# Kernel optimization log

Measured on AMD Instinct MI355X. Metric: run time of the kernel, lower is better.

The kernel has to match this reference:

```python
import jax, jax.numpy as jnp
import numpy as np
from jax import lax

S = 8  # down/up-sample factor


def _seg_means(x, z):
    """Directional running means between zero-boundaries along the last axis.

    x: float [..., L] values; z: bool [..., L], True at zero-boundary positions.
    For position t strictly between consecutive boundaries (prev, nxt):
      lr[t] = mean(x[prev:t+1]),  rl[t] = mean(x[t:nxt+1]); else keep x[t].
    """
    L = x.shape[-1]
    ar = jnp.arange(L)
    ax = x.ndim - 1
    # last zero index strictly before t (-1 if none)
    idx = jnp.where(z, ar, -1)
    prev = lax.cummax(idx, axis=ax)
    prev = jnp.concatenate(
        [jnp.full(prev.shape[:-1] + (1,), -1, prev.dtype), prev[..., :-1]], axis=-1)
    # first zero index strictly after t (L if none)
    idx2 = jnp.where(z, ar, L)
    nxt = lax.cummin(idx2, axis=ax, reverse=True)
    nxt = jnp.concatenate(
        [nxt[..., 1:], jnp.full(nxt.shape[:-1] + (1,), L, nxt.dtype)], axis=-1)
    valid = (~z) & (prev >= 0) & (nxt < L)
    # padded cumsum: cs0[..., k] = sum(x[..., :k]), length L+1
    cs0 = jnp.concatenate(
        [jnp.zeros(x.shape[:-1] + (1,), x.dtype), jnp.cumsum(x, axis=-1)], axis=-1)
    prev_c = jnp.clip(prev, 0, L - 1)
    nxt_c = jnp.clip(nxt, 0, L - 1)
    sum_lr = cs0[..., 1:] - jnp.take_along_axis(cs0, prev_c, axis=-1)   # x[prev..t]
    sum_rl = jnp.take_along_axis(cs0, nxt_c + 1, axis=-1) - cs0[..., :-1]  # x[t..nxt]
    cnt_lr = jnp.maximum(ar - prev + 1, 1).astype(x.dtype)
    cnt_rl = jnp.maximum(nxt - ar + 1, 1).astype(x.dtype)
    lr = jnp.where(valid, sum_lr / cnt_lr, x)
    rl = jnp.where(valid, sum_rl / cnt_rl, x)
    return lr, rl


def setup_inputs() -> dict:
    key = jax.random.key(0)
    k0, k1 = jax.random.split(key)
    N, C, H, W = 8, 1, 2048, 2048
    x0 = jax.random.normal(k0, (N, C, H, W), dtype=jnp.float32)
    x1 = jax.random.randint(k1, (N, C, H, W), 0, 8, dtype=jnp.int32)
    return {"x0": x0, "x1": x1}


def reference(x0, x1):
    # nearest-neighbor downsample by 8 (matches F.interpolate scale_factor=1/8, mode='nearest')
    x0d = x0[..., ::S, ::S]
    zd = (x1[..., ::S, ::S] == 0)
    # horizontal pass (along rows)
    xh_lr, xh_rl = _seg_means(x0d, zd)
    # vertical pass (along columns) via transpose
    xv_tb, xv_bt = _seg_means(jnp.swapaxes(x0d, -1, -2), jnp.swapaxes(zd, -1, -2))
    y = xh_lr + xh_rl + jnp.swapaxes(xv_tb, -1, -2) + jnp.swapaxes(xv_bt, -1, -2)
    # nearest-neighbor upsample by 8
    y = jnp.repeat(jnp.repeat(y, S, axis=-2), S, axis=-1)
    return y
```

## Files before the change

### kernel.cpp

```cpp
#include <hip/hip_runtime.h>

#define DS   256
#define FULL 2048
#define NIMG 8
#define CG   4

typedef float f32x4 __attribute__((ext_vector_type(4)));
typedef int   i32x4 __attribute__((ext_vector_type(4)));

__device__ __forceinline__ float seg_fast(float x, bool z, int j,
                                          float* s_cs,
                                          unsigned long long* s_msk,
                                          float* s_ws) {
    const int lane = j & 63;
    const int w    = j >> 6;
    unsigned long long m = __ballot(z);

    float s = x;
    #pragma unroll
    for (int off = 1; off < 64; off <<= 1) {
        float t = __shfl_up(s, off, 64);
        if (lane >= off) s += t;
    }
    if (lane == 63) s_ws[w]  = s;
    if (lane == 0)  s_msk[w] = m;
    __syncthreads();

    float pre = 0.f;
    for (int ww = 0; ww < w; ++ww) pre += s_ws[ww];
    s += pre;
    s_cs[j] = s;

    unsigned long long lo = m & ((1ULL << lane) - 1ULL);
    int prev = -1;
    if (lo) prev = (w << 6) + 63 - __builtin_clzll(lo);
    else {
        for (int ww = w - 1; ww >= 0; --ww) {
            unsigned long long mm = s_msk[ww];
            if (mm) { prev = (ww << 6) + 63 - __builtin_clzll(mm); break; }
        }
    }
    unsigned long long hi = m & ~((2ULL << lane) - 1ULL);
    int nxt = DS;
    if (hi) nxt = (w << 6) + __builtin_ctzll(hi);
    else {
        for (int ww = w + 1; ww < 4; ++ww) {
            unsigned long long mm = s_msk[ww];
            if (mm) { nxt = (ww << 6) + __builtin_ctzll(mm); break; }
        }
    }
    __syncthreads();

    bool valid = (!z) && (prev >= 0) && (nxt < DS);
    if (valid) {
        float cs_j   = s_cs[j];
        float cs_pm1 = (prev > 0) ? s_cs[prev - 1] : 0.f;
        float cs_n   = s_cs[nxt];
        float cs_jm1 = (j > 0) ? s_cs[j - 1] : 0.f;
        return (cs_j - cs_pm1) / (float)(j - prev + 1)
             + (cs_n - cs_jm1) / (float)(nxt - j + 1);
    }
    return 2.f * x;
}

__global__ __launch_bounds__(256) void k_row(const float* __restrict__ x0,
                                             const int* __restrict__ x1,
                                             float2* __restrict__ xz,
                                             float* __restrict__ yH) {
    __shared__ float s_xf[DS];
    __shared__ float s_zf[DS];
    __shared__ float s_cs[DS];
    __shared__ unsigned long long s_msk[4];
    __shared__ float s_ws[4];
    const int j = threadIdx.x;
    const int line = blockIdx.x;
    const int n = line >> 8, i = line & 255;

    const float* rb0 = x0 + (size_t)(n * FULL + i * 8) * FULL;
    const int*   rb1 = x1 + (size_t)(n * FULL + i * 8) * FULL;
    f32x4 a0 = *(const f32x4*)(rb0 + 4 * j);
    f32x4 a1 = *(const f32x4*)(rb0 + 1024 + 4 * j);
    i32x4 b0 = *(const i32x4*)(rb1 + 4 * j);
    i32x4 b1 = *(const i32x4*)(rb1 + 1024 + 4 * j);
    if (!(j & 1)) {
        int s0 = (j >> 1);
        int s1 = 128 + (j >> 1);
        s_xf[s0] = a0[0];  s_zf[s0] = (b0[0] == 0) ? 1.f : 0.f;
        s_xf[s1] = a1[0];  s_zf[s1] = (b1[0] == 0) ? 1.f : 0.f;
    }
    __syncthreads();

    float x = s_xf[j];
    bool  z = (s_zf[j] != 0.f);
    float r = seg_fast(x, z, j, s_cs, s_msk, s_ws);

    yH[(line << 8) + j] = r;
    xz[(line << 8) + j] = make_float2(x, z ? 1.f : 0.f);
}

__global__ __launch_bounds__(256) void k_col(const float2* __restrict__ xz,
                                             float* __restrict__ yH) {
    __shared__ float s_x[CG][DS];
    __shared__ float s_z[CG][DS];
    __shared__ float s_y[CG][DS];
    __shared__ float s_cs[DS];
    __shared__ unsigned long long s_msk[4];
    __shared__ float s_ws[4];
    const int t = threadIdx.x;
    const int g = blockIdx.x;
    const int n = g >> 6, c0 = (g & 63) * CG;

    const float2* base = xz + (n << 16) + (t << 8) + c0;
    f32x4 v0 = *(const f32x4*)(base);
    f32x4 v1 = *(const f32x4*)(base + 2);
    s_x[0][t] = v0[0]; s_z[0][t] = v0[1];
    s_x[1][t] = v0[2]; s_z[1][t] = v0[3];
    s_x[2][t] = v1[0]; s_z[2][t] = v1[1];
    s_x[3][t] = v1[2]; s_z[3][t] = v1[3];

    #pragma unroll
    for (int c = 0; c < CG; ++c) {
        float x = s_x[c][t];
        bool  z = (s_z[c][t] != 0.f);
        s_y[c][t] = seg_fast(x, z, t, s_cs, s_msk, s_ws);
    }

    float* dst = yH + (n << 16) + (t << 8) + c0;
    f32x4 acc = *(const f32x4*)dst;
    acc[0] += s_y[0][t]; acc[1] += s_y[1][t];
    acc[2] += s_y[2][t]; acc[3] += s_y[3][t];
    *(f32x4*)dst = acc;
}

__global__ __launch_bounds__(256) void k_up(const float* __restrict__ yH,
                                            f32x4* __restrict__ out) {
    int gid = blockIdx.x * 256 + threadIdx.x;
    int g2  = gid << 1;
    int j4  = g2 & 511;
    int r   = g2 >> 9;
    int I   = r & 2047;
    int n   = r >> 11;
    float v = yH[(n << 16) + ((I >> 3) << 8) + (j4 >> 1)];
    f32x4 vv = { v, v, v, v };
    out[g2]     = vv;
    out[g2 + 1] = vv;
}

extern "C" void kernel_launch(void* const* d_in, const int* in_sizes, int n_in,
                              void* d_out, int out_size, void* d_ws, size_t ws_size,
                              hipStream_t stream) {
    const float* x0 = (const float*)d_in[0];
    const int*   x1 = (const int*)d_in[1];
    f32x4* out = (f32x4*)d_out;

    float2* xz = (float2*)d_ws;
    float*  yH = (float*)(xz + NIMG * DS * DS);

    dim3 blk(256);
    k_row<<<dim3(NIMG * DS),      blk, 0, stream>>>(x0, x1, xz, yH);
    k_col<<<dim3(NIMG * DS / CG), blk, 0, stream>>>(xz, yH);
    k_up <<<dim3(16384),          blk, 0, stream>>>(yH, out);
}
```

Baseline: 48.89 us.

## Fuse column pass with upsample and use nontemporal loads/stores

Merges the column segment-mean kernel with the nearest-neighbour upsample so each block adds the horizontal result, stages the four columns in shared memory, and writes the 8x8 upsampled tiles directly. This removes one launch and the read-modify-write of the intermediate plus its reread. Input loads in the row kernel and output stores use nontemporal hints. The large output write is now issued by only 512 blocks, which may limit memory parallelism.

```diff
diff --git a/kernel.cpp b/kernel.cpp
--- a/kernel.cpp
+++ b/kernel.cpp
@@ -78,10 +78,10 @@
 
     const float* rb0 = x0 + (size_t)(n * FULL + i * 8) * FULL;
     const int*   rb1 = x1 + (size_t)(n * FULL + i * 8) * FULL;
-    f32x4 a0 = *(const f32x4*)(rb0 + 4 * j);
-    f32x4 a1 = *(const f32x4*)(rb0 + 1024 + 4 * j);
-    i32x4 b0 = *(const i32x4*)(rb1 + 4 * j);
-    i32x4 b1 = *(const i32x4*)(rb1 + 1024 + 4 * j);
+    f32x4 a0 = __builtin_nontemporal_load((const f32x4*)(rb0 + 4 * j));
+    f32x4 a1 = __builtin_nontemporal_load((const f32x4*)(rb0 + 1024 + 4 * j));
+    i32x4 b0 = __builtin_nontemporal_load((const i32x4*)(rb1 + 4 * j));
+    i32x4 b1 = __builtin_nontemporal_load((const i32x4*)(rb1 + 1024 + 4 * j));
     if (!(j & 1)) {
         int s0 = (j >> 1);
         int s1 = 128 + (j >> 1);
@@ -98,11 +98,12 @@
     xz[(line << 8) + j] = make_float2(x, z ? 1.f : 0.f);
 }
 
-__global__ __launch_bounds__(256) void k_col(const float2* __restrict__ xz,
-                                             float* __restrict__ yH) {
+__global__ __launch_bounds__(256) void k_colup(const float2* __restrict__ xz,
+                                               const float* __restrict__ yH,
+                                               f32x4* __restrict__ out) {
     __shared__ float s_x[CG][DS];
     __shared__ float s_z[CG][DS];
-    __shared__ float s_y[CG][DS];
+    __shared__ float s_out[CG][DS + 1];
     __shared__ float s_cs[DS];
     __shared__ unsigned long long s_msk[4];
     __shared__ float s_ws[4];
@@ -113,6 +114,7 @@
     const float2* base = xz + (n << 16) + (t << 8) + c0;
     f32x4 v0 = *(const f32x4*)(base);
     f32x4 v1 = *(const f32x4*)(base + 2);
+    f32x4 h  = *(const f32x4*)(yH + (n << 16) + (t << 8) + c0);
     s_x[0][t] = v0[0]; s_z[0][t] = v0[1];
     s_x[1][t] = v0[2]; s_z[1][t] = v0[3];
     s_x[2][t] = v1[0]; s_z[2][t] = v1[1];
@@ -122,28 +124,21 @@
     for (int c = 0; c < CG; ++c) {
         float x = s_x[c][t];
         bool  z = (s_z[c][t] != 0.f);
-        s_y[c][t] = seg_fast(x, z, t, s_cs, s_msk, s_ws);
+        float r = seg_fast(x, z, t, s_cs, s_msk, s_ws);
+        s_out[c][t] = r + h[c];
     }
+    __syncthreads();
 
-    float* dst = yH + (n << 16) + (t << 8) + c0;
-    f32x4 acc = *(const f32x4*)dst;
-    acc[0] += s_y[0][t]; acc[1] += s_y[1][t];
-    acc[2] += s_y[2][t]; acc[3] += s_y[3][t];
-    *(f32x4*)dst = acc;
-}
-
-__global__ __launch_bounds__(256) void k_up(const float* __restrict__ yH,
-                                            f32x4* __restrict__ out) {
-    int gid = blockIdx.x * 256 + threadIdx.x;
-    int g2  = gid << 1;
-    int j4  = g2 & 511;
-    int r   = g2 >> 9;
-    int I   = r & 2047;
-    int n   = r >> 11;
-    float v = yH[(n << 16) + ((I >> 3) << 8) + (j4 >> 1)];
-    f32x4 vv = { v, v, v, v };
-    out[g2]     = vv;
-    out[g2 + 1] = vv;
+    f32x4* ob = out + ((size_t)n << 20) + (c0 << 1);
+    #pragma unroll 4
+    for (int k = 0; k < 64; ++k) {
+        int idx = (k << 8) + t;
+        int I   = idx >> 3;
+        int s   = idx & 7;
+        float v = s_out[s >> 1][I >> 3];
+        f32x4 vv = { v, v, v, v };
+        __builtin_nontemporal_store(vv, ob + (size_t)I * 512 + s);
+    }
 }
 
 extern "C" void kernel_launch(void* const* d_in, const int* in_sizes, int n_in,
@@ -157,7 +152,6 @@
     float*  yH = (float*)(xz + NIMG * DS * DS);
 
     dim3 blk(256);
-    k_row<<<dim3(NIMG * DS),      blk, 0, stream>>>(x0, x1, xz, yH);
-    k_col<<<dim3(NIMG * DS / CG), blk, 0, stream>>>(xz, yH);
-    k_up <<<dim3(16384),          blk, 0, stream>>>(yH, out);
+    k_row  <<<dim3(NIMG * DS),      blk, 0, stream>>>(x0, x1, xz, yH);
+    k_colup<<<dim3(NIMG * DS / CG), blk, 0, stream>>>(xz, yH, out);
 }
```

Result: faster. 47.10 us (-3.7%).
